# Performance work log

Hardware: AMD Instinct MI355X
Metric: run time of the kernel (lower is better)

Reference implementation:

```python
import jax, jax.numpy as jnp
import numpy as np

DIM = 768
NUM_HEADS = 12
HEAD_DIM = DIM // NUM_HEADS
SCALE = HEAD_DIM ** -0.5


def setup_inputs() -> dict:
    key = jax.random.key(0)
    k_x, k_qw, k_qb, k_pw, k_pb = jax.random.split(key, 5)
    B, N = 4, 2048
    x = jax.random.normal(k_x, (B, N, DIM), dtype=jnp.float32)
    s = 1.0 / np.sqrt(DIM)
    qkv_w = jax.random.normal(k_qw, (3 * DIM, DIM), dtype=jnp.float32) * s
    qkv_b = jax.random.normal(k_qb, (3 * DIM,), dtype=jnp.float32) * 0.02
    proj_w = jax.random.normal(k_pw, (DIM, DIM), dtype=jnp.float32) * s
    proj_b = jax.random.normal(k_pb, (DIM,), dtype=jnp.float32) * 0.02
    return {"x": x, "qkv_w": qkv_w, "qkv_b": qkv_b, "proj_w": proj_w, "proj_b": proj_b}


def reference(x, qkv_w, qkv_b, proj_w, proj_b):
    B, N, D = x.shape
    H, Hd = NUM_HEADS, HEAD_DIM
    # qkv linear: [B,N,3D] -> [3,B,H,N,Hd]
    qkv = (x @ qkv_w.T + qkv_b).reshape(B, N, 3, H, Hd).transpose(2, 0, 3, 1, 4)
    q, k, v = qkv[0], qkv[1], qkv[2]
    scores = jnp.einsum("bhnd,bhmd->bhnm", q, k) * SCALE  # [B,H,N,N]
    attn = jax.nn.softmax(scores, axis=-1)
    out = jnp.einsum("bhnm,bhmd->bhnd", attn, v)  # [B,H,N,Hd]
    out = out.transpose(0, 2, 1, 3).reshape(B, N, D)
    return out @ proj_w.T + proj_b
```

## Files before the change

kernel.cpp:

```cpp
#include <hip/hip_runtime.h>

#define SEQ 2048
#define NB 4
#define NH 12
#define DHEAD 64
#define DMODEL 768
#define D3 2304
#define MTOT 8192
#define QSCALE 0.18033688011112042f

typedef float f4v __attribute__((ext_vector_type(4)));
typedef float fl4 __attribute__((ext_vector_type(4)));
typedef short s8v __attribute__((ext_vector_type(8)));
typedef __bf16 b8v __attribute__((ext_vector_type(8)));
typedef unsigned int ui4 __attribute__((ext_vector_type(4)));
typedef unsigned int ui2 __attribute__((ext_vector_type(2)));
typedef unsigned short us4 __attribute__((ext_vector_type(4)));

#define GLDS16(g, l)                                                            \
  __builtin_amdgcn_global_load_lds(                                             \
      (const __attribute__((address_space(1))) void*)(g),                       \
      (__attribute__((address_space(3))) void*)(l), 16, 0, 0)

template <typename T>
__device__ inline auto mfma_try(T a, T b, f4v c, int)
    -> decltype(__builtin_amdgcn_mfma_f32_16x16x32_bf16(a, b, c, 0, 0, 0)) {
  return __builtin_amdgcn_mfma_f32_16x16x32_bf16(a, b, c, 0, 0, 0);
}
template <typename T>
__device__ inline f4v mfma_try(T a, T b, f4v c, long) {
  return __builtin_amdgcn_mfma_f32_16x16x32_bf16(
      __builtin_bit_cast(b8v, a), __builtin_bit_cast(b8v, b), c, 0, 0, 0);
}
__device__ inline f4v mfma16(s8v a, s8v b, f4v c) { return mfma_try(a, b, c, 0); }

__device__ inline unsigned short f2bf(float f) {
  union { float f; unsigned u; } v; v.f = f;
  unsigned r = v.u + 0x7FFFu + ((v.u >> 16) & 1u);
  return (unsigned short)(r >> 16);
}

__device__ inline unsigned pack2(float a, float b) {
  unsigned ua = __builtin_bit_cast(unsigned, a) + 0x8000u;
  unsigned ub = __builtin_bit_cast(unsigned, b) + 0x8000u;
  return __builtin_amdgcn_perm(ub, ua, 0x07060302u);
}

__global__ void k_f2bf(const float* __restrict__ in, unsigned short* __restrict__ out, int n4) {
  int i = blockIdx.x * 256 + threadIdx.x;
  if (i >= n4) return;
  fl4 f = ((const fl4*)in)[i];
  us4 o;
  o[0] = f2bf(f[0]); o[1] = f2bf(f[1]); o[2] = f2bf(f[2]); o[3] = f2bf(f[3]);
  ((us4*)out)[i] = o;
}

template <int EPI>
__global__ __launch_bounds__(256, 4) void k_gemm_nt(
    const unsigned short* __restrict__ A,
    const unsigned short* __restrict__ Bm,
    const float* __restrict__ bias,
    float* __restrict__ outF,
    unsigned short* __restrict__ outQ,
    unsigned short* __restrict__ outK,
    unsigned short* __restrict__ outV,
    int K) {
  __shared__ unsigned short As[128 * 64];
  __shared__ unsigned short Bs[128 * 64];
  const int tid = threadIdx.x;
  const int lane = tid & 63;
  const int wave = tid >> 6;
  const int wr = wave >> 1, wc = wave & 1;
  const int lr = lane & 15;
  const int lq = lane >> 4;
  const int rowBase = blockIdx.y * 128;
  const int colBase = blockIdx.x * 128;

  f4v acc[4][4];
#pragma unroll
  for (int i = 0; i < 4; ++i)
#pragma unroll
    for (int j = 0; j < 4; ++j) acc[i][j] = f4v{0.f, 0.f, 0.f, 0.f};

  const int srow = wave * 8 + (lane >> 3);
  const int scol = ((lane & 7) ^ ((lane >> 3) & 7)) * 8;
  const unsigned short* Ag0 = A + (long)(rowBase + srow) * K + scol;
  const unsigned short* Bg0 = Bm + (long)(colBase + srow) * K + scol;
  unsigned short* Al0 = &As[srow * 64 + (lane & 7) * 8];
  unsigned short* Bl0 = &Bs[srow * 64 + (lane & 7) * 8];
  const int kTiles = K >> 6;
  const int swz = (lr & 7);

  for (int kt = 0; kt < kTiles; ++kt) {
#pragma unroll
    for (int p = 0; p < 4; ++p) {
      GLDS16(Ag0 + kt * 64 + p * 32 * K, Al0 + p * 32 * 64);
      GLDS16(Bg0 + kt * 64 + p * 32 * K, Bl0 + p * 32 * 64);
    }
    __syncthreads();
#pragma unroll
    for (int ks = 0; ks < 2; ++ks) {
      s8v af[4], bf[4];
#pragma unroll
      for (int i = 0; i < 4; ++i)
        af[i] = *(const s8v*)&As[(wr * 64 + i * 16 + lr) * 64 + ((ks * 4 + lq) ^ swz) * 8];
#pragma unroll
      for (int j = 0; j < 4; ++j)
        bf[j] = *(const s8v*)&Bs[(wc * 64 + j * 16 + lr) * 64 + ((ks * 4 + lq) ^ swz) * 8];
#pragma unroll
      for (int i = 0; i < 4; ++i)
#pragma unroll
        for (int j = 0; j < 4; ++j) acc[i][j] = mfma16(af[i], bf[j], acc[i][j]);
    }
    __syncthreads();
  }

#pragma unroll
  for (int j = 0; j < 4; ++j) {
    const int col = colBase + wc * 64 + j * 16 + lr;
    const float bv = bias[col];
    if (EPI == 1) {
#pragma unroll
      for (int i = 0; i < 4; ++i)
#pragma unroll
        for (int e = 0; e < 4; ++e) {
          const int row = rowBase + wr * 64 + i * 16 + lq * 4 + e;
          outF[row * DMODEL + col] = acc[i][j][e] + bv;
        }
    } else {
      const int t = col / DMODEL;
      const int h = (col >> 6) % NH;
      const int hd = col & 63;
#pragma unroll
      for (int i = 0; i < 4; ++i) {
        const int row = rowBase + wr * 64 + i * 16 + lq * 4;
        const int b = row >> 11;
        const int n = row & 2047;
        if (t == 2) {
          float v0 = acc[i][j][0] + bv, v1 = acc[i][j][1] + bv;
          float v2 = acc[i][j][2] + bv, v3 = acc[i][j][3] + bv;
          *(ui2*)&outV[(((b * NH + h) * DHEAD) + hd) * SEQ + n] =
              ui2{pack2(v0, v1), pack2(v2, v3)};
        } else {
#pragma unroll
          for (int e = 0; e < 4; ++e) {
            const float v = acc[i][j][e] + bv;
            if (t == 0)
              outQ[(((b * NH + h) * SEQ) + n + e) * DHEAD + hd] = f2bf(v * QSCALE);
            else
              outK[(((b * NH + h) * SEQ) + n + e) * DHEAD + hd] = f2bf(v);
          }
        }
      }
    }
  }
}

__global__ __launch_bounds__(256, 3) void k_attn(
    const unsigned short* __restrict__ Q,
    const unsigned short* __restrict__ Kg,
    const unsigned short* __restrict__ Vt,
    unsigned short* __restrict__ Ob) {
  __shared__ unsigned short Ks[128 * 64];
  __shared__ unsigned short Vs[64 * 136];
  const int tid = threadIdx.x;
  const int lane = tid & 63;
  const int wave = tid >> 6;
  const int lr = lane & 15;
  const int lq = lane >> 4;
  const int bh = blockIdx.y;
  const int b = bh / NH, h = bh % NH;
  const int q0 = blockIdx.x * 128;
  const unsigned short* Qb = Q + (long)bh * SEQ * DHEAD;
  const unsigned short* Kb = Kg + (long)bh * SEQ * DHEAD;
  const unsigned short* Vb = Vt + (long)bh * DHEAD * SEQ;

  s8v qf[2][2];
#pragma unroll
  for (int i = 0; i < 2; ++i)
#pragma unroll
    for (int ss = 0; ss < 2; ++ss)
      qf[i][ss] = *(const s8v*)(Qb + (q0 + wave * 32 + i * 16 + lr) * DHEAD + ss * 32 + lq * 8);

  f4v o[2][4];
  f4v la[2] = {f4v{0.f, 0.f, 0.f, 0.f}, f4v{0.f, 0.f, 0.f, 0.f}};
  const f4v zc = f4v{0.f, 0.f, 0.f, 0.f};
  const s8v ones = {0x3F80, 0x3F80, 0x3F80, 0x3F80, 0x3F80, 0x3F80, 0x3F80, 0x3F80};
#pragma unroll
  for (int i = 0; i < 2; ++i)
#pragma unroll
    for (int jo = 0; jo < 4; ++jo) o[i][jo] = f4v{0.f, 0.f, 0.f, 0.f};

  const int srow = wave * 8 + (lane >> 3);
  const int scol = ((lane & 7) ^ ((lane >> 3) & 7)) * 8;
  const unsigned short* Kg0 = Kb + (long)srow * DHEAD + scol;
  unsigned short* Kl0 = &Ks[srow * 64 + (lane & 7) * 8];
  const int swz = (lr & 7);
  const int rv = tid >> 4;
  const int cc = tid & 15;
  const int ssS = cc >> 2;
  const int st1 = ((cc & 1) << 4) | ((cc & 2) << 1);

  for (int kt = 0; kt < SEQ / 128; ++kt) {
#pragma unroll
    for (int p = 0; p < 4; ++p)
      GLDS16(Kg0 + (long)(kt * 128 + p * 32) * DHEAD, Kl0 + p * 32 * 64);
#pragma unroll
    for (int p = 0; p < 4; ++p) {
      ui4 vv = *(const ui4*)(Vb + (long)(rv + p * 16) * SEQ + kt * 128 + cc * 8);
      *(ui2*)&Vs[(rv + p * 16) * 136 + ssS * 32 + st1] = ui2{vv[0], vv[1]};
      *(ui2*)&Vs[(rv + p * 16) * 136 + ssS * 32 + st1 + 8] = ui2{vv[2], vv[3]};
    }
    __syncthreads();

    f4v s[2][8];
#pragma unroll
    for (int t = 0; t < 8; ++t) {
      s8v kf0 = *(const s8v*)&Ks[(t * 16 + lr) * 64 + ((0 * 4 + lq) ^ swz) * 8];
      s8v kf1 = *(const s8v*)&Ks[(t * 16 + lr) * 64 + ((1 * 4 + lq) ^ swz) * 8];
      s[0][t] = mfma16(kf0, qf[0][0], zc);
      s[1][t] = mfma16(kf0, qf[1][0], zc);
      s[0][t] = mfma16(kf1, qf[0][1], s[0][t]);
      s[1][t] = mfma16(kf1, qf[1][1], s[1][t]);
    }

    unsigned pk[2][8][2];
#pragma unroll
    for (int i = 0; i < 2; ++i)
#pragma unroll
      for (int t = 0; t < 8; ++t) {
        float p0 = exp2f(s[i][t][0]);
        float p1 = exp2f(s[i][t][1]);
        float p2 = exp2f(s[i][t][2]);
        float p3 = exp2f(s[i][t][3]);
        pk[i][t][0] = pack2(p0, p1);
        pk[i][t][1] = pack2(p2, p3);
      }

#pragma unroll
    for (int ss = 0; ss < 4; ++ss) {
      s8v vf[4];
#pragma unroll
      for (int jo = 0; jo < 4; ++jo)
        vf[jo] = *(const s8v*)&Vs[(jo * 16 + lr) * 136 + ss * 32 + lq * 8];
#pragma unroll
      for (int i = 0; i < 2; ++i) {
        s8v pf = __builtin_bit_cast(
            s8v, ui4{pk[i][2 * ss][0], pk[i][2 * ss][1], pk[i][2 * ss + 1][0], pk[i][2 * ss + 1][1]});
        la[i] = mfma16(ones, pf, la[i]);
#pragma unroll
        for (int jo = 0; jo < 4; ++jo) o[i][jo] = mfma16(vf[jo], pf, o[i][jo]);
      }
    }
    __syncthreads();
  }

  float linv[2];
  linv[0] = 1.0f / la[0][0];
  linv[1] = 1.0f / la[1][0];

#pragma unroll
  for (int i = 0; i < 2; ++i) {
    const long nrow = (long)(b * SEQ + q0 + wave * 32 + i * 16 + lr) * DMODEL;
#pragma unroll
    for (int jo = 0; jo < 4; ++jo) {
      float v0 = o[i][jo][0] * linv[i];
      float v1 = o[i][jo][1] * linv[i];
      float v2 = o[i][jo][2] * linv[i];
      float v3 = o[i][jo][3] * linv[i];
      *(ui2*)(Ob + nrow + h * DHEAD + jo * 16 + lq * 4) = ui2{pack2(v0, v1), pack2(v2, v3)};
    }
  }
}

extern "C" void kernel_launch(void* const* d_in, const int* in_sizes, int n_in,
                              void* d_out, int out_size, void* d_ws, size_t ws_size,
                              hipStream_t stream) {
  (void)in_sizes; (void)n_in; (void)out_size; (void)ws_size;
  const float* x = (const float*)d_in[0];
  const float* qkv_w = (const float*)d_in[1];
  const float* qkv_b = (const float*)d_in[2];
  const float* proj_w = (const float*)d_in[3];
  const float* proj_b = (const float*)d_in[4];
  float* out = (float*)d_out;

  unsigned short* ws = (unsigned short*)d_ws;
  unsigned short* xb = ws;
  unsigned short* wqkvb = xb + 6291456;
  unsigned short* wprjb = wqkvb + 1769472;
  unsigned short* qb = wprjb + 589824;
  unsigned short* kb = qb + 6291456;
  unsigned short* vtb = kb + 6291456;
  unsigned short* aob = vtb + 6291456;

  k_f2bf<<<(6291456 / 4 + 255) / 256, 256, 0, stream>>>(x, xb, 6291456 / 4);
  k_f2bf<<<(1769472 / 4 + 255) / 256, 256, 0, stream>>>(qkv_w, wqkvb, 1769472 / 4);
  k_f2bf<<<(589824 / 4 + 255) / 256, 256, 0, stream>>>(proj_w, wprjb, 589824 / 4);

  k_gemm_nt<0><<<dim3(D3 / 128, MTOT / 128), 256, 0, stream>>>(
      xb, wqkvb, qkv_b, nullptr, qb, kb, vtb, DMODEL);
  k_attn<<<dim3(SEQ / 128, NB * NH), 256, 0, stream>>>(qb, kb, vtb, aob);
  k_gemm_nt<1><<<dim3(DMODEL / 128, MTOT / 128), 256, 0, stream>>>(
      aob, wprjb, proj_b, out, nullptr, nullptr, nullptr, DMODEL);
}
```

Measured before the change: 244.0 us.

## Fuse conversion kernels, async-load pre-permuted V, use hardware exp2, retune gemm bounds

Merges the three fp32-to-bf16 conversion launches into one kernel. The QKV epilogue now writes V in a pre-permuted column order, so the attention kernel can stage V through global_load_lds with an XOR swizzle instead of register loads and scattered LDS stores. It also swaps exp2f for the raw hardware v_exp_f32 and lowers the GEMM launch-bounds occupancy hint from 4 to 3. The aim is fewer launches, less V staging overhead and cheaper exponentials. The risks are slightly lower exp accuracy and a permutation that must exactly match the mfma fragment order.

```diff
diff --git a/kernel.cpp b/kernel.cpp
--- a/kernel.cpp
+++ b/kernel.cpp
@@ -22,6 +22,16 @@
       (const __attribute__((address_space(1))) void*)(g),                       \
       (__attribute__((address_space(3))) void*)(l), 16, 0, 0)
 
+__device__ inline float fast_exp2(float x) {
+#if __has_builtin(__builtin_amdgcn_exp2f)
+  return __builtin_amdgcn_exp2f(x);
+#else
+  float r;
+  asm("v_exp_f32 %0, %1" : "=v"(r) : "v"(x));
+  return r;
+#endif
+}
+
 template <typename T>
 __device__ inline auto mfma_try(T a, T b, f4v c, int)
     -> decltype(__builtin_amdgcn_mfma_f32_16x16x32_bf16(a, b, c, 0, 0, 0)) {
@@ -46,17 +56,28 @@
   return __builtin_amdgcn_perm(ub, ua, 0x07060302u);
 }
 
-__global__ void k_f2bf(const float* __restrict__ in, unsigned short* __restrict__ out, int n4) {
+#define NX4 1572864
+#define NW14 442368
+#define NW24 147456
+__global__ void k_cvt(const float* __restrict__ x, const float* __restrict__ w1,
+                      const float* __restrict__ w2, unsigned short* __restrict__ ox,
+                      unsigned short* __restrict__ o1, unsigned short* __restrict__ o2) {
   int i = blockIdx.x * 256 + threadIdx.x;
-  if (i >= n4) return;
-  fl4 f = ((const fl4*)in)[i];
+  const float* src;
+  unsigned short* dst;
+  int off;
+  if (i < NX4) { src = x; dst = ox; off = i; }
+  else if (i < NX4 + NW14) { src = w1; dst = o1; off = i - NX4; }
+  else if (i < NX4 + NW14 + NW24) { src = w2; dst = o2; off = i - NX4 - NW14; }
+  else return;
+  fl4 f = ((const fl4*)src)[off];
   us4 o;
   o[0] = f2bf(f[0]); o[1] = f2bf(f[1]); o[2] = f2bf(f[2]); o[3] = f2bf(f[3]);
-  ((us4*)out)[i] = o;
+  ((us4*)dst)[off] = o;
 }
 
 template <int EPI>
-__global__ __launch_bounds__(256, 4) void k_gemm_nt(
+__global__ __launch_bounds__(256, 3) void k_gemm_nt(
     const unsigned short* __restrict__ A,
     const unsigned short* __restrict__ Bm,
     const float* __restrict__ bias,
@@ -137,9 +158,11 @@
         const int b = row >> 11;
         const int n = row & 2047;
         if (t == 2) {
+          const int bq = (n >> 2) & 7;
+          const int np = (n & ~31) + ((bq & 3) << 3) + ((bq >> 2) << 2);
           float v0 = acc[i][j][0] + bv, v1 = acc[i][j][1] + bv;
           float v2 = acc[i][j][2] + bv, v3 = acc[i][j][3] + bv;
-          *(ui2*)&outV[(((b * NH + h) * DHEAD) + hd) * SEQ + n] =
+          *(ui2*)&outV[(((b * NH + h) * DHEAD) + hd) * SEQ + np] =
               ui2{pack2(v0, v1), pack2(v2, v3)};
         } else {
 #pragma unroll
@@ -162,7 +185,7 @@
     const unsigned short* __restrict__ Vt,
     unsigned short* __restrict__ Ob) {
   __shared__ unsigned short Ks[128 * 64];
-  __shared__ unsigned short Vs[64 * 136];
+  __shared__ unsigned short Vs[64 * 128];
   const int tid = threadIdx.x;
   const int lane = tid & 63;
   const int wave = tid >> 6;
@@ -196,21 +219,18 @@
   const unsigned short* Kg0 = Kb + (long)srow * DHEAD + scol;
   unsigned short* Kl0 = &Ks[srow * 64 + (lane & 7) * 8];
   const int swz = (lr & 7);
-  const int rv = tid >> 4;
-  const int cc = tid & 15;
-  const int ssS = cc >> 2;
-  const int st1 = ((cc & 1) << 4) | ((cc & 2) << 1);
+  const int vdrow = wave * 4 + (lane >> 4);
+  const int vchunk = (lane & 15) ^ vdrow;
+  const unsigned short* Vg0 = Vb + (long)vdrow * SEQ + vchunk * 8;
+  unsigned short* Vl0 = &Vs[vdrow * 128 + (lane & 15) * 8];
 
   for (int kt = 0; kt < SEQ / 128; ++kt) {
 #pragma unroll
     for (int p = 0; p < 4; ++p)
       GLDS16(Kg0 + (long)(kt * 128 + p * 32) * DHEAD, Kl0 + p * 32 * 64);
 #pragma unroll
-    for (int p = 0; p < 4; ++p) {
-      ui4 vv = *(const ui4*)(Vb + (long)(rv + p * 16) * SEQ + kt * 128 + cc * 8);
-      *(ui2*)&Vs[(rv + p * 16) * 136 + ssS * 32 + st1] = ui2{vv[0], vv[1]};
-      *(ui2*)&Vs[(rv + p * 16) * 136 + ssS * 32 + st1 + 8] = ui2{vv[2], vv[3]};
-    }
+    for (int p = 0; p < 4; ++p)
+      GLDS16(Vg0 + (long)(p * 16) * SEQ + kt * 128, Vl0 + p * 16 * 128);
     __syncthreads();
 
     f4v s[2][8];
@@ -229,10 +249,10 @@
     for (int i = 0; i < 2; ++i)
 #pragma unroll
       for (int t = 0; t < 8; ++t) {
-        float p0 = exp2f(s[i][t][0]);
-        float p1 = exp2f(s[i][t][1]);
-        float p2 = exp2f(s[i][t][2]);
-        float p3 = exp2f(s[i][t][3]);
+        float p0 = fast_exp2(s[i][t][0]);
+        float p1 = fast_exp2(s[i][t][1]);
+        float p2 = fast_exp2(s[i][t][2]);
+        float p3 = fast_exp2(s[i][t][3]);
         pk[i][t][0] = pack2(p0, p1);
         pk[i][t][1] = pack2(p2, p3);
       }
@@ -242,7 +262,7 @@
       s8v vf[4];
 #pragma unroll
       for (int jo = 0; jo < 4; ++jo)
-        vf[jo] = *(const s8v*)&Vs[(jo * 16 + lr) * 136 + ss * 32 + lq * 8];
+        vf[jo] = *(const s8v*)&Vs[(jo * 16 + lr) * 128 + ((ss * 4 + lq) ^ lr) * 8];
 #pragma unroll
       for (int i = 0; i < 2; ++i) {
         s8v pf = __builtin_bit_cast(
@@ -293,9 +313,8 @@
   unsigned short* vtb = kb + 6291456;
   unsigned short* aob = vtb + 6291456;
 
-  k_f2bf<<<(6291456 / 4 + 255) / 256, 256, 0, stream>>>(x, xb, 6291456 / 4);
-  k_f2bf<<<(1769472 / 4 + 255) / 256, 256, 0, stream>>>(qkv_w, wqkvb, 1769472 / 4);
-  k_f2bf<<<(589824 / 4 + 255) / 256, 256, 0, stream>>>(proj_w, wprjb, 589824 / 4);
+  k_cvt<<<(NX4 + NW14 + NW24 + 255) / 256, 256, 0, stream>>>(
+      x, qkv_w, proj_w, xb, wqkvb, wprjb);
 
   k_gemm_nt<0><<<dim3(D3 / 128, MTOT / 128), 256, 0, stream>>>(
       xb, wqkvb, qkv_b, nullptr, qb, kb, vtb, DMODEL);
```

After: 208.8 us. 14.4% less time.
